# Kernel tuning notes

Measured on AMD Instinct MI355X. Metric: run time of the kernel, lower is better.

The kernel has to match this reference:

```python
import jax, jax.numpy as jnp
import numpy as np

N = 100000   # n_nodes
E = 800000   # n_edges
IN = 128
HID = 128
OUT = 40
EPS = 1e-5   # BatchNorm1d eps


def setup_inputs() -> dict:
    key = jax.random.key(0)
    ks = jax.random.split(key, 16)
    def w(k, i, o):
        return jax.random.normal(k, (i, o), jnp.float32) / np.sqrt(i).astype(np.float32)
    return {
        "x": jax.random.normal(ks[0], (N, IN), jnp.float32),
        "edge_index": jax.random.randint(ks[1], (2, E), 0, N, dtype=jnp.int64),
        # SAGEConv weights: Wl acts on aggregated neighbors, Wr on root features
        "Wl0": w(ks[2], IN, HID),  "Wr0": w(ks[3], IN, HID),
        "Wl1": w(ks[4], HID, HID), "Wr1": w(ks[5], HID, HID),
        "Wl2": w(ks[6], HID, OUT), "Wr2": w(ks[7], HID, OUT),
        "b2": jnp.zeros((OUT,), jnp.float32),  # bias only on last layer
        # BatchNorm params for layers 0,1 (last layer has no BN)
        "g0": jnp.ones((HID,), jnp.float32), "be0": jnp.zeros((HID,), jnp.float32),
        "g1": jnp.ones((HID,), jnp.float32), "be1": jnp.zeros((HID,), jnp.float32),
    }


def _sage_conv(x, src, dst, Wl, Wr, b=None):
    # mean aggregation of source messages at destination nodes
    msg = x[src]                                             # [E, d] gather
    agg = jax.ops.segment_sum(msg, dst, num_segments=N)      # [N, d]
    cnt = jax.ops.segment_sum(jnp.ones((src.shape[0],), x.dtype), dst,
                              num_segments=N)                # [N]
    mean = agg / jnp.maximum(cnt, 1.0)[:, None]
    out = mean @ Wl + x @ Wr
    if b is not None:
        out = out + b
    return out


def _batch_norm(h, gamma, beta):
    # training-mode BN over node dim, biased variance (matches torch BatchNorm1d)
    mu = h.mean(axis=0)
    var = h.var(axis=0)
    return (h - mu) * jax.lax.rsqrt(var + EPS) * gamma + beta


def reference(x, edge_index, Wl0, Wr0, Wl1, Wr1, Wl2, Wr2, b2, g0, be0, g1, be1):
    src, dst = edge_index[0], edge_index[1]
    h = _sage_conv(x, src, dst, Wl0, Wr0)
    h = jax.nn.relu(_batch_norm(h, g0, be0))
    h = _sage_conv(h, src, dst, Wl1, Wr1)
    h = jax.nn.relu(_batch_norm(h, g1, be1))
    h = _sage_conv(h, src, dst, Wl2, Wr2, b2)
    return h
```

## Files before the change

kernel.cpp:

```cpp
#include <hip/hip_runtime.h>
#include <hip/hip_bf16.h>

#define N_NODES 100000
#define N_EDGES 800000
#define EPS 1e-5f
#define NBANK 32
#define HB_BLOCKS 256
#define HB_PER 3125
#define CS_GPB 64
#define BUCKET_N 12500
#define MROW 68

typedef __attribute__((ext_vector_type(8))) short short8;
typedef __attribute__((ext_vector_type(4))) float floatx4;

__device__ __forceinline__ unsigned short f2b(float f) {
    unsigned int u = __float_as_uint(f);
    u = (u + 0x7fffu + ((u >> 16) & 1u)) >> 16;
    return (unsigned short)u;
}
__device__ __forceinline__ float blo(unsigned int u) { return __uint_as_float(u << 16); }
__device__ __forceinline__ float bhi(unsigned int u) { return __uint_as_float(u & 0xffff0000u); }

__global__ void cvt_f32_bf16(const float* __restrict__ x, unsigned short* __restrict__ o, int n4) {
    int i = blockIdx.x * blockDim.x + threadIdx.x;
    if (i >= n4) return;
    float4 v = ((const float4*)x)[i];
    ushort4 r;
    r.x = f2b(v.x); r.y = f2b(v.y); r.z = f2b(v.z); r.w = f2b(v.w);
    ((ushort4*)o)[i] = r;
}

__global__ void pack_w(const float* __restrict__ Wl, const float* __restrict__ Wr,
                       unsigned short* __restrict__ out, int Hreal, int NCT) {
    int tid = blockIdx.x * blockDim.x + threadIdx.x;
    int total = NCT * 8 * 64 * 8;
    if (tid >= total) return;
    int i = tid & 7;
    int lane = (tid >> 3) & 63;
    int q = tid >> 9;
    int c = q % NCT;
    int t = q / NCT;
    int k = t * 32 + (lane >> 4) * 8 + i;
    int n = c * 16 + (lane & 15);
    float v = 0.f;
    if (n < Hreal) v = (k < 128) ? Wl[k * Hreal + n] : Wr[(k - 128) * Hreal + n];
    out[tid] = f2b(v);
}

__global__ void __launch_bounds__(256) hist_k(const int* __restrict__ dst,
                                              unsigned int* __restrict__ cnt,
                                              unsigned int* __restrict__ bhist) {
    __shared__ unsigned int lh[8];
    if (threadIdx.x < 8) lh[threadIdx.x] = 0;
    __syncthreads();
    int start = blockIdx.x * HB_PER;
    for (int i = threadIdx.x; i < HB_PER; i += 256) {
        int d = dst[start + i];
        atomicAdd(&cnt[d], 1u);
        atomicAdd(&lh[(unsigned int)d / BUCKET_N], 1u);
    }
    __syncthreads();
    if (threadIdx.x < 8) bhist[threadIdx.x * HB_BLOCKS + blockIdx.x] = lh[threadIdx.x];
}

__global__ void bscan(unsigned int* __restrict__ A) {
    __shared__ unsigned int part[256];
    int t = threadIdx.x;
    unsigned int v[8];
    unsigned int s = 0;
#pragma unroll
    for (int i = 0; i < 8; i++) { v[i] = A[t * 8 + i]; s += v[i]; }
    part[t] = s; __syncthreads();
    for (int off = 1; off < 256; off <<= 1) {
        unsigned int add = (t >= off) ? part[t - off] : 0u;
        __syncthreads();
        part[t] += add;
        __syncthreads();
    }
    unsigned int base = part[t] - s;
#pragma unroll
    for (int i = 0; i < 8; i++) { unsigned int old = v[i]; A[t * 8 + i] = base; base += old; }
}

__global__ void __launch_bounds__(256) bscatter(const int* __restrict__ src,
                                                const int* __restrict__ dst,
                                                const unsigned int* __restrict__ boffs,
                                                unsigned int* __restrict__ ebuf) {
    __shared__ unsigned int cur[8];
    if (threadIdx.x < 8) cur[threadIdx.x] = boffs[threadIdx.x * HB_BLOCKS + blockIdx.x];
    __syncthreads();
    int start = blockIdx.x * HB_PER;
    for (int i = threadIdx.x; i < HB_PER; i += 256) {
        int d = dst[start + i];
        int s = src[start + i];
        unsigned int b = (unsigned int)d / BUCKET_N;
        unsigned int dl = (unsigned int)d - b * BUCKET_N;
        unsigned int pos = atomicAdd(&cur[b], 1u);
        ebuf[pos] = (unsigned int)s | (dl << 17);
    }
}

__global__ void __launch_bounds__(256) cscatter(const unsigned int* __restrict__ ebuf,
                                                const unsigned int* __restrict__ rowptr,
                                                unsigned int* __restrict__ cursor,
                                                int* __restrict__ srclist) {
    int g = blockIdx.x & 7;
    int gblk = blockIdx.x >> 3;
    unsigned int estart = rowptr[g * BUCKET_N];
    unsigned int eend = (g == 7) ? N_EDGES : rowptr[(g + 1) * BUCKET_N];
    unsigned int nume = eend - estart;
    unsigned int per = (nume + CS_GPB - 1) / CS_GPB;
    unsigned int s0 = estart + gblk * per;
    unsigned int s1 = s0 + per; if (s1 > eend) s1 = eend;
    unsigned int nodebase = g * BUCKET_N;
    for (unsigned int i = s0 + threadIdx.x; i < s1; i += 256) {
        unsigned int p = ebuf[i];
        unsigned int s = p & 0x1FFFFu;
        unsigned int node = nodebase + (p >> 17);
        unsigned int pos = atomicAdd(&cursor[node], 1u);
        srclist[pos] = (int)s;
    }
}

__global__ void scan1(const unsigned int* __restrict__ cnt, unsigned int* __restrict__ rowptr,
                      unsigned int* __restrict__ bsum) {
    __shared__ unsigned int sh[256];
    int t = threadIdx.x;
    int i = blockIdx.x * 256 + t;
    unsigned int v = (i < N_NODES) ? cnt[i] : 0u;
    sh[t] = v; __syncthreads();
    for (int off = 1; off < 256; off <<= 1) {
        unsigned int add = (t >= off) ? sh[t - off] : 0u;
        __syncthreads();
        sh[t] += add;
        __syncthreads();
    }
    if (i < N_NODES) rowptr[i] = sh[t] - v;
    if (t == 255) bsum[blockIdx.x] = sh[255];
}

__global__ void scan2(const unsigned int* __restrict__ bsum, unsigned int* __restrict__ boff, int nb) {
    __shared__ unsigned int sh[512];
    int t = threadIdx.x;
    unsigned int v = (t < nb) ? bsum[t] : 0u;
    sh[t] = v; __syncthreads();
    for (int off = 1; off < 512; off <<= 1) {
        unsigned int add = (t >= off) ? sh[t - off] : 0u;
        __syncthreads();
        sh[t] += add;
        __syncthreads();
    }
    if (t < nb) boff[t] = sh[t] - v;
}

__global__ void scan3(unsigned int* __restrict__ rowptr, const unsigned int* __restrict__ boff,
                      unsigned int* __restrict__ cursor) {
    int i = blockIdx.x * 256 + threadIdx.x;
    if (i < N_NODES) {
        unsigned int r = rowptr[i] + boff[blockIdx.x];
        rowptr[i] = r;
        cursor[i] = r;
    }
    if (i == N_NODES) rowptr[N_NODES] = N_EDGES;
}

__device__ __forceinline__ void agg_phase16(const unsigned short* __restrict__ hb,
                                            const unsigned int* __restrict__ rowptr,
                                            const int* __restrict__ srclist,
                                            unsigned int* __restrict__ smean,
                                            int wave, int g, int l, int blockrow) {
    const uint4* hp = (const uint4*)hb;
    int nl = wave * 4 + g;
    int node = blockrow + nl;
    float f0 = 0.f, f1 = 0.f, f2 = 0.f, f3 = 0.f, f4 = 0.f, f5 = 0.f, f6 = 0.f, f7 = 0.f;
    unsigned int b = rowptr[node], e = rowptr[node + 1];
    unsigned int p = b;
    for (; p + 4 <= e; p += 4) {
        int s0 = srclist[p];
        int s1 = srclist[p + 1];
        int s2 = srclist[p + 2];
        int s3 = srclist[p + 3];
        uint4 u0 = hp[(size_t)s0 * 16 + l];
        uint4 u1 = hp[(size_t)s1 * 16 + l];
        uint4 u2 = hp[(size_t)s2 * 16 + l];
        uint4 u3 = hp[(size_t)s3 * 16 + l];
        f0 += blo(u0.x); f1 += bhi(u0.x); f2 += blo(u0.y); f3 += bhi(u0.y);
        f4 += blo(u0.z); f5 += bhi(u0.z); f6 += blo(u0.w); f7 += bhi(u0.w);
        f0 += blo(u1.x); f1 += bhi(u1.x); f2 += blo(u1.y); f3 += bhi(u1.y);
        f4 += blo(u1.z); f5 += bhi(u1.z); f6 += blo(u1.w); f7 += bhi(u1.w);
        f0 += blo(u2.x); f1 += bhi(u2.x); f2 += blo(u2.y); f3 += bhi(u2.y);
        f4 += blo(u2.z); f5 += bhi(u2.z); f6 += blo(u2.w); f7 += bhi(u2.w);
        f0 += blo(u3.x); f1 += bhi(u3.x); f2 += blo(u3.y); f3 += bhi(u3.y);
        f4 += blo(u3.z); f5 += bhi(u3.z); f6 += blo(u3.w); f7 += bhi(u3.w);
    }
    if (p + 2 <= e) {
        int s0 = srclist[p];
        int s1 = srclist[p + 1];
        uint4 u0 = hp[(size_t)s0 * 16 + l];
        uint4 u1 = hp[(size_t)s1 * 16 + l];
        f0 += blo(u0.x); f1 += bhi(u0.x); f2 += blo(u0.y); f3 += bhi(u0.y);
        f4 += blo(u0.z); f5 += bhi(u0.z); f6 += blo(u0.w); f7 += bhi(u0.w);
        f0 += blo(u1.x); f1 += bhi(u1.x); f2 += blo(u1.y); f3 += bhi(u1.y);
        f4 += blo(u1.z); f5 += bhi(u1.z); f6 += blo(u1.w); f7 += bhi(u1.w);
        p += 2;
    }
    if (p < e) {
        int s0 = srclist[p];
        uint4 u0 = hp[(size_t)s0 * 16 + l];
        f0 += blo(u0.x); f1 += bhi(u0.x); f2 += blo(u0.y); f3 += bhi(u0.y);
        f4 += blo(u0.z); f5 += bhi(u0.z); f6 += blo(u0.w); f7 += bhi(u0.w);
    }
    unsigned int deg = e - b;
    float r = 1.0f / (float)(deg > 1u ? deg : 1u);
    uint4 o;
    o.x = (unsigned int)f2b(f0 * r) | ((unsigned int)f2b(f1 * r) << 16);
    o.y = (unsigned int)f2b(f2 * r) | ((unsigned int)f2b(f3 * r) << 16);
    o.z = (unsigned int)f2b(f4 * r) | ((unsigned int)f2b(f5 * r) << 16);
    o.w = (unsigned int)f2b(f6 * r) | ((unsigned int)f2b(f7 * r) << 16);
    *(uint4*)&smean[nl * MROW + l * 4] = o;
}

__global__ void __launch_bounds__(256) gemm2f_k(const unsigned short* __restrict__ hb,
                                                const unsigned int* __restrict__ rowptr,
                                                const int* __restrict__ srclist,
                                                const unsigned short* __restrict__ Bp,
                                                unsigned short* __restrict__ outb,
                                                float* __restrict__ sums) {
    __shared__ unsigned int smean[16 * MROW];
    __shared__ float lds_s[128];
    __shared__ float lds_s2[128];
    int wave = threadIdx.x >> 6;
    int lane = threadIdx.x & 63;
    int quad = lane >> 4;
    int l15 = lane & 15;
    int blockrow = blockIdx.x * 16;

    if (threadIdx.x < 128) { lds_s[threadIdx.x] = 0.f; lds_s2[threadIdx.x] = 0.f; }

    agg_phase16(hb, rowptr, srclist, smean, wave, quad, l15, blockrow);
    __syncthreads();

    floatx4 acc[2];
    acc[0] = (floatx4){0.f, 0.f, 0.f, 0.f};
    acc[1] = (floatx4){0.f, 0.f, 0.f, 0.f};

    int r0 = blockrow + l15;

#pragma unroll
    for (int t = 0; t < 8; t++) {
        short8 a0;
        if (t < 4) {
            a0 = *(const short8*)&smean[l15 * MROW + t * 16 + quad * 4];
        } else {
            int koff = (t & 3) * 32 + quad * 8;
            a0 = *(const short8*)(hb + (size_t)r0 * 128 + koff);
        }
#pragma unroll
        for (int c = 0; c < 2; c++) {
            int cidx = wave * 2 + c;
            short8 bf = *(const short8*)(Bp + ((size_t)(t * 8 + cidx) * 64 + lane) * 8);
            acc[c] = __builtin_amdgcn_mfma_f32_16x16x32_bf16(a0, bf, acc[c], 0, 0, 0);
        }
    }

#pragma unroll
    for (int c = 0; c < 2; c++) {
        int col = wave * 32 + c * 16 + l15;
        float s = 0.f, s2 = 0.f;
#pragma unroll
        for (int r = 0; r < 4; r++) {
            int row = blockrow + quad * 4 + r;
            float v = acc[c][r];
            outb[(size_t)row * 128 + col] = f2b(v);
            s += v; s2 += v * v;
        }
        s += __shfl_xor(s, 16);  s += __shfl_xor(s, 32);
        s2 += __shfl_xor(s2, 16); s2 += __shfl_xor(s2, 32);
        if (quad == 0) {
            atomicAdd(&lds_s[col], s);
            atomicAdd(&lds_s2[col], s2);
        }
    }

    __syncthreads();
    if (threadIdx.x < 128) {
        int bank = blockIdx.x & (NBANK - 1);
        atomicAdd(&sums[bank * 256 + threadIdx.x], lds_s[threadIdx.x]);
        atomicAdd(&sums[bank * 256 + 128 + threadIdx.x], lds_s2[threadIdx.x]);
    }
}

__global__ void __launch_bounds__(256) gemm3f_k(const unsigned short* __restrict__ hb,
                                                const unsigned int* __restrict__ rowptr,
                                                const int* __restrict__ srclist,
                                                const unsigned short* __restrict__ Bp,
                                                const float* __restrict__ bias,
                                                float* __restrict__ out) {
    __shared__ unsigned int smean[16 * MROW];
    int wave = threadIdx.x >> 6;
    int lane = threadIdx.x & 63;
    int quad = lane >> 4;
    int l15 = lane & 15;
    int blockrow = blockIdx.x * 16;

    agg_phase16(hb, rowptr, srclist, smean, wave, quad, l15, blockrow);
    __syncthreads();

    if (wave >= 3) return;

    floatx4 acc = (floatx4){0.f, 0.f, 0.f, 0.f};
    int r0 = blockrow + l15;

#pragma unroll
    for (int t = 0; t < 8; t++) {
        short8 a0;
        if (t < 4) {
            a0 = *(const short8*)&smean[l15 * MROW + t * 16 + quad * 4];
        } else {
            int koff = (t & 3) * 32 + quad * 8;
            a0 = *(const short8*)(hb + (size_t)r0 * 128 + koff);
        }
        short8 bf = *(const short8*)(Bp + ((size_t)(t * 3 + wave) * 64 + lane) * 8);
        acc = __builtin_amdgcn_mfma_f32_16x16x32_bf16(a0, bf, acc, 0, 0, 0);
    }

    int col = wave * 16 + l15;
    if (col < 40) {
#pragma unroll
        for (int r = 0; r < 4; r++) {
            int row = blockrow + quad * 4 + r;
            out[(size_t)row * 40 + col] = acc[r] + bias[col];
        }
    }
}

__global__ void bn_finalize(const float* __restrict__ sums, const float* __restrict__ g,
                            const float* __restrict__ be, float* __restrict__ sc,
                            float* __restrict__ sh) {
    __shared__ float lds[256];
    int t = threadIdx.x;
    float s = 0.f;
#pragma unroll 8
    for (int bk = 0; bk < NBANK; bk++) s += sums[bk * 256 + t];
    lds[t] = s;
    __syncthreads();
    if (t < 128) {
        float inv_n = 1.0f / (float)N_NODES;
        float mu = lds[t] * inv_n;
        float var = lds[128 + t] * inv_n - mu * mu;
        float sf = g[t] * rsqrtf(var + EPS);
        sc[t] = sf;
        sh[t] = be[t] - mu * sf;
    }
}

__global__ void bn_apply(const unsigned int* __restrict__ Cb, const float* __restrict__ sc,
                         const float* __restrict__ sh, unsigned short* __restrict__ ho) {
    int i = blockIdx.x * 256 + threadIdx.x;
    if (i >= N_NODES * 16) return;
    uint4 v = ((const uint4*)Cb)[i];
    int c0 = (i * 8) & 127;
    uint4 o;
    float e0 = fmaxf(0.f, blo(v.x) * sc[c0 + 0] + sh[c0 + 0]);
    float e1 = fmaxf(0.f, bhi(v.x) * sc[c0 + 1] + sh[c0 + 1]);
    float e2 = fmaxf(0.f, blo(v.y) * sc[c0 + 2] + sh[c0 + 2]);
    float e3 = fmaxf(0.f, bhi(v.y) * sc[c0 + 3] + sh[c0 + 3]);
    float e4 = fmaxf(0.f, blo(v.z) * sc[c0 + 4] + sh[c0 + 4]);
    float e5 = fmaxf(0.f, bhi(v.z) * sc[c0 + 5] + sh[c0 + 5]);
    float e6 = fmaxf(0.f, blo(v.w) * sc[c0 + 6] + sh[c0 + 6]);
    float e7 = fmaxf(0.f, bhi(v.w) * sc[c0 + 7] + sh[c0 + 7]);
    o.x = (unsigned int)f2b(e0) | ((unsigned int)f2b(e1) << 16);
    o.y = (unsigned int)f2b(e2) | ((unsigned int)f2b(e3) << 16);
    o.z = (unsigned int)f2b(e4) | ((unsigned int)f2b(e5) << 16);
    o.w = (unsigned int)f2b(e6) | ((unsigned int)f2b(e7) << 16);
    ((uint4*)ho)[i] = o;
}

extern "C" void kernel_launch(void* const* d_in, const int* in_sizes, int n_in,
                              void* d_out, int out_size, void* d_ws, size_t ws_size,
                              hipStream_t stream) {
    const float* x   = (const float*)d_in[0];
    const int* ei    = (const int*)d_in[1];
    const float* Wl0 = (const float*)d_in[2];
    const float* Wr0 = (const float*)d_in[3];
    const float* Wl1 = (const float*)d_in[4];
    const float* Wr1 = (const float*)d_in[5];
    const float* Wl2 = (const float*)d_in[6];
    const float* Wr2 = (const float*)d_in[7];
    const float* b2  = (const float*)d_in[8];
    const float* g0  = (const float*)d_in[9];
    const float* be0 = (const float*)d_in[10];
    const float* g1  = (const float*)d_in[11];
    const float* be1 = (const float*)d_in[12];

    char* ws = (char*)d_ws;
    size_t off = 0;
    auto alloc = [&](size_t bytes) -> void* {
        void* p = ws + off;
        off += (bytes + 4095) & ~(size_t)4095;
        return p;
    };

    const size_t NB16 = (size_t)N_NODES * 128 * 2;
    unsigned short* xb   = (unsigned short*)alloc(NB16);
    unsigned short* h1   = (unsigned short*)alloc(NB16);
    unsigned short* C    = (unsigned short*)alloc(NB16);
    unsigned int* cnt    = (unsigned int*)alloc((size_t)N_NODES * 4);
    unsigned int* rowptr = (unsigned int*)alloc((size_t)(N_NODES + 1) * 4);
    unsigned int* cursor = (unsigned int*)alloc((size_t)N_NODES * 4);
    int* srclist         = (int*)alloc((size_t)N_EDGES * 4);
    unsigned int* ebuf   = (unsigned int*)alloc((size_t)N_EDGES * 4);
    unsigned int* bhist  = (unsigned int*)alloc(8 * HB_BLOCKS * 4);
    unsigned int* bsum   = (unsigned int*)alloc(512 * 4);
    unsigned int* boff   = (unsigned int*)alloc(512 * 4);
    float* sums0         = (float*)alloc(NBANK * 256 * 4);
    float* sums1         = (float*)alloc(NBANK * 256 * 4);
    float* sc            = (float*)alloc(128 * 4);
    float* sh            = (float*)alloc(128 * 4);
    unsigned short* W0p  = (unsigned short*)alloc(8 * 8 * 64 * 8 * 2);
    unsigned short* W1p  = (unsigned short*)alloc(8 * 8 * 64 * 8 * 2);
    unsigned short* W2p  = (unsigned short*)alloc(3 * 8 * 64 * 8 * 2);
    unsigned short* h2   = xb;

    const int* srcp = ei;
    const int* dstp = ei + N_EDGES;

    hipMemsetAsync(cnt, 0, (size_t)N_NODES * 4, stream);
    hipMemsetAsync(sums0, 0, (size_t)2 * NBANK * 256 * 4, stream);
    cvt_f32_bf16<<<12500, 256, 0, stream>>>(x, xb, N_NODES * 32);
    pack_w<<<(8 * 4096 + 255) / 256, 256, 0, stream>>>(Wl0, Wr0, W0p, 128, 8);
    pack_w<<<(8 * 4096 + 255) / 256, 256, 0, stream>>>(Wl1, Wr1, W1p, 128, 8);
    pack_w<<<(3 * 4096 + 255) / 256, 256, 0, stream>>>(Wl2, Wr2, W2p, 40, 3);

    hist_k<<<HB_BLOCKS, 256, 0, stream>>>(dstp, cnt, bhist);
    scan1<<<391, 256, 0, stream>>>(cnt, rowptr, bsum);
    scan2<<<1, 512, 0, stream>>>(bsum, boff, 391);
    scan3<<<391, 256, 0, stream>>>(rowptr, boff, cursor);
    bscan<<<1, 256, 0, stream>>>(bhist);
    bscatter<<<HB_BLOCKS, 256, 0, stream>>>(srcp, dstp, bhist, ebuf);
    cscatter<<<8 * CS_GPB, 256, 0, stream>>>(ebuf, rowptr, cursor, srclist);

    gemm2f_k<<<6250, 256, 0, stream>>>(xb, rowptr, srclist, W0p, C, sums0);
    bn_finalize<<<1, 256, 0, stream>>>(sums0, g0, be0, sc, sh);
    bn_apply<<<6250, 256, 0, stream>>>((const unsigned int*)C, sc, sh, h1);

    gemm2f_k<<<6250, 256, 0, stream>>>(h1, rowptr, srclist, W1p, C, sums1);
    bn_finalize<<<1, 256, 0, stream>>>(sums1, g1, be1, sc, sh);
    bn_apply<<<6250, 256, 0, stream>>>((const unsigned int*)C, sc, sh, h2);

    gemm3f_k<<<6250, 256, 0, stream>>>(h2, rowptr, srclist, W2p, b2, (float*)d_out);

    (void)in_sizes; (void)n_in; (void)out_size; (void)ws_size;
}
```

Baseline: 372.1 us.

## Balance neighbor aggregation by splitting block edges evenly across lane groups

The mean aggregation now gives each 16-lane group an equal slice of the block's 16-node edge range instead of one destination node per group. The local destination index is packed into the upper bits of srclist, so partial sums can be flushed with LDS float atomics into a per-block fp32 accumulator before normalisation and the bf16 conversion. This targets the load imbalance from skewed node degrees, where one group with many edges stalls the whole block. In exchange it adds an LDS zeroing pass, an extra barrier, shuffles to broadcast edge indices, and LDS atomic traffic at each destination change.

```diff
diff --git a/kernel.cpp b/kernel.cpp
--- a/kernel.cpp
+++ b/kernel.cpp
@@ -10,6 +10,7 @@
 #define CS_GPB 64
 #define BUCKET_N 12500
 #define MROW 68
+#define ACC_S 132
 
 typedef __attribute__((ext_vector_type(8))) short short8;
 typedef __attribute__((ext_vector_type(4))) float floatx4;
@@ -119,7 +120,7 @@
         unsigned int s = p & 0x1FFFFu;
         unsigned int node = nodebase + (p >> 17);
         unsigned int pos = atomicAdd(&cursor[node], 1u);
-        srclist[pos] = (int)s;
+        srclist[pos] = (int)(s | ((node & 15u) << 17));
     }
 }
 
@@ -168,57 +169,91 @@
 __device__ __forceinline__ void agg_phase16(const unsigned short* __restrict__ hb,
                                             const unsigned int* __restrict__ rowptr,
                                             const int* __restrict__ srclist,
+                                            float* __restrict__ accf,
                                             unsigned int* __restrict__ smean,
-                                            int wave, int g, int l, int blockrow) {
+                                            int blockrow) {
+    const int tid = threadIdx.x;
+    const int g = tid >> 4;
+    const int l = tid & 15;
+    const int srcbase = (g & 3) << 4;
+
+    for (int i = tid; i < 16 * ACC_S; i += 256) accf[i] = 0.f;
+    __syncthreads();
+
+    unsigned int e0 = rowptr[blockrow];
+    unsigned int e1 = rowptr[blockrow + 16];
+    unsigned int nE = e1 - e0;
+    unsigned int per = (nE + 15u) >> 4;
+    unsigned int start = e0 + (unsigned int)g * per;
+    unsigned int end = start + per;
+    if (end > e1) end = e1;
+
     const uint4* hp = (const uint4*)hb;
-    int nl = wave * 4 + g;
-    int node = blockrow + nl;
     float f0 = 0.f, f1 = 0.f, f2 = 0.f, f3 = 0.f, f4 = 0.f, f5 = 0.f, f6 = 0.f, f7 = 0.f;
-    unsigned int b = rowptr[node], e = rowptr[node + 1];
-    unsigned int p = b;
-    for (; p + 4 <= e; p += 4) {
-        int s0 = srclist[p];
-        int s1 = srclist[p + 1];
-        int s2 = srclist[p + 2];
-        int s3 = srclist[p + 3];
-        uint4 u0 = hp[(size_t)s0 * 16 + l];
-        uint4 u1 = hp[(size_t)s1 * 16 + l];
-        uint4 u2 = hp[(size_t)s2 * 16 + l];
-        uint4 u3 = hp[(size_t)s3 * 16 + l];
-        f0 += blo(u0.x); f1 += bhi(u0.x); f2 += blo(u0.y); f3 += bhi(u0.y);
-        f4 += blo(u0.z); f5 += bhi(u0.z); f6 += blo(u0.w); f7 += bhi(u0.w);
-        f0 += blo(u1.x); f1 += bhi(u1.x); f2 += blo(u1.y); f3 += bhi(u1.y);
-        f4 += blo(u1.z); f5 += bhi(u1.z); f6 += blo(u1.w); f7 += bhi(u1.w);
-        f0 += blo(u2.x); f1 += bhi(u2.x); f2 += blo(u2.y); f3 += bhi(u2.y);
-        f4 += blo(u2.z); f5 += bhi(u2.z); f6 += blo(u2.w); f7 += bhi(u2.w);
-        f0 += blo(u3.x); f1 += bhi(u3.x); f2 += blo(u3.y); f3 += bhi(u3.y);
-        f4 += blo(u3.z); f5 += bhi(u3.z); f6 += blo(u3.w); f7 += bhi(u3.w);
-    }
-    if (p + 2 <= e) {
-        int s0 = srclist[p];
-        int s1 = srclist[p + 1];
-        uint4 u0 = hp[(size_t)s0 * 16 + l];
-        uint4 u1 = hp[(size_t)s1 * 16 + l];
-        f0 += blo(u0.x); f1 += bhi(u0.x); f2 += blo(u0.y); f3 += bhi(u0.y);
-        f4 += blo(u0.z); f5 += bhi(u0.z); f6 += blo(u0.w); f7 += bhi(u0.w);
-        f0 += blo(u1.x); f1 += bhi(u1.x); f2 += blo(u1.y); f3 += bhi(u1.y);
-        f4 += blo(u1.z); f5 += bhi(u1.z); f6 += blo(u1.w); f7 += bhi(u1.w);
-        p += 2;
-    }
-    if (p < e) {
-        int s0 = srclist[p];
-        uint4 u0 = hp[(size_t)s0 * 16 + l];
-        f0 += blo(u0.x); f1 += bhi(u0.x); f2 += blo(u0.y); f3 += bhi(u0.y);
-        f4 += blo(u0.z); f5 += bhi(u0.z); f6 += blo(u0.w); f7 += bhi(u0.w);
-    }
-    unsigned int deg = e - b;
-    float r = 1.0f / (float)(deg > 1u ? deg : 1u);
-    uint4 o;
-    o.x = (unsigned int)f2b(f0 * r) | ((unsigned int)f2b(f1 * r) << 16);
-    o.y = (unsigned int)f2b(f2 * r) | ((unsigned int)f2b(f3 * r) << 16);
-    o.z = (unsigned int)f2b(f4 * r) | ((unsigned int)f2b(f5 * r) << 16);
-    o.w = (unsigned int)f2b(f6 * r) | ((unsigned int)f2b(f7 * r) << 16);
-    *(uint4*)&smean[nl * MROW + l * 4] = o;
+    int dcur = -1;
+
+#define ACC8(U) { f0 += blo(U.x); f1 += bhi(U.x); f2 += blo(U.y); f3 += bhi(U.y); \
+                  f4 += blo(U.z); f5 += bhi(U.z); f6 += blo(U.w); f7 += bhi(U.w); }
+#define FLUSHA() { if (dcur >= 0) { float* ap = accf + dcur * ACC_S + l * 8; \
+    atomicAdd(&ap[(0 + l) & 7], f0); atomicAdd(&ap[(1 + l) & 7], f1); \
+    atomicAdd(&ap[(2 + l) & 7], f2); atomicAdd(&ap[(3 + l) & 7], f3); \
+    atomicAdd(&ap[(4 + l) & 7], f4); atomicAdd(&ap[(5 + l) & 7], f5); \
+    atomicAdd(&ap[(6 + l) & 7], f6); atomicAdd(&ap[(7 + l) & 7], f7); \
+    f0 = f1 = f2 = f3 = f4 = f5 = f6 = f7 = 0.f; } }
+#define EDGE(P, U) { int dd = (int)((P >> 17) & 15u); \
+    if (dd != dcur) { FLUSHA(); dcur = dd; } ACC8(U); }
+
+    for (unsigned int base = start; base < end; base += 16u) {
+        unsigned int rem = end - base;
+        int m = rem < 16u ? (int)rem : 16;
+        unsigned int pk = 0u;
+        if ((unsigned int)l < rem) pk = (unsigned int)srclist[base + (unsigned int)l];
+        int j = 0;
+        for (; j + 4 <= m; j += 4) {
+            unsigned int p0 = (unsigned int)__shfl((int)pk, srcbase + j + 0);
+            unsigned int p1 = (unsigned int)__shfl((int)pk, srcbase + j + 1);
+            unsigned int p2 = (unsigned int)__shfl((int)pk, srcbase + j + 2);
+            unsigned int p3 = (unsigned int)__shfl((int)pk, srcbase + j + 3);
+            uint4 u0 = hp[(size_t)(p0 & 0x1FFFFu) * 16 + l];
+            uint4 u1 = hp[(size_t)(p1 & 0x1FFFFu) * 16 + l];
+            uint4 u2 = hp[(size_t)(p2 & 0x1FFFFu) * 16 + l];
+            uint4 u3 = hp[(size_t)(p3 & 0x1FFFFu) * 16 + l];
+            EDGE(p0, u0); EDGE(p1, u1); EDGE(p2, u2); EDGE(p3, u3);
+        }
+        for (; j < m; ++j) {
+            unsigned int p0 = (unsigned int)__shfl((int)pk, srcbase + j);
+            uint4 u0 = hp[(size_t)(p0 & 0x1FFFFu) * 16 + l];
+            EDGE(p0, u0);
+        }
+    }
+    FLUSHA();
+#undef EDGE
+#undef FLUSHA
+#undef ACC8
+
+    __syncthreads();
+
+    {
+        unsigned int b = rowptr[blockrow + g];
+        unsigned int e = rowptr[blockrow + g + 1];
+        unsigned int deg = e - b;
+        float r = 1.0f / (float)(deg > 1u ? deg : 1u);
+        const float* ap = accf + g * ACC_S + l * 8;
+        float v0 = ap[(0 + l) & 7] * r;
+        float v1 = ap[(1 + l) & 7] * r;
+        float v2 = ap[(2 + l) & 7] * r;
+        float v3 = ap[(3 + l) & 7] * r;
+        float v4 = ap[(4 + l) & 7] * r;
+        float v5 = ap[(5 + l) & 7] * r;
+        float v6 = ap[(6 + l) & 7] * r;
+        float v7 = ap[(7 + l) & 7] * r;
+        uint4 o;
+        o.x = (unsigned int)f2b(v0) | ((unsigned int)f2b(v1) << 16);
+        o.y = (unsigned int)f2b(v2) | ((unsigned int)f2b(v3) << 16);
+        o.z = (unsigned int)f2b(v4) | ((unsigned int)f2b(v5) << 16);
+        o.w = (unsigned int)f2b(v6) | ((unsigned int)f2b(v7) << 16);
+        *(uint4*)&smean[g * MROW + l * 4] = o;
+    }
 }
 
 __global__ void __launch_bounds__(256) gemm2f_k(const unsigned short* __restrict__ hb,
@@ -227,6 +262,7 @@
                                                 const unsigned short* __restrict__ Bp,
                                                 unsigned short* __restrict__ outb,
                                                 float* __restrict__ sums) {
+    __shared__ float accf[16 * ACC_S];
     __shared__ unsigned int smean[16 * MROW];
     __shared__ float lds_s[128];
     __shared__ float lds_s2[128];
@@ -238,7 +274,7 @@
 
     if (threadIdx.x < 128) { lds_s[threadIdx.x] = 0.f; lds_s2[threadIdx.x] = 0.f; }
 
-    agg_phase16(hb, rowptr, srclist, smean, wave, quad, l15, blockrow);
+    agg_phase16(hb, rowptr, srclist, accf, smean, blockrow);
     __syncthreads();
 
     floatx4 acc[2];
@@ -297,6 +333,7 @@
                                                 const unsigned short* __restrict__ Bp,
                                                 const float* __restrict__ bias,
                                                 float* __restrict__ out) {
+    __shared__ float accf[16 * ACC_S];
     __shared__ unsigned int smean[16 * MROW];
     int wave = threadIdx.x >> 6;
     int lane = threadIdx.x & 63;
@@ -304,7 +341,7 @@
     int l15 = lane & 15;
     int blockrow = blockIdx.x * 16;
 
-    agg_phase16(hb, rowptr, srclist, smean, wave, quad, l15, blockrow);
+    agg_phase16(hb, rowptr, srclist, accf, smean, blockrow);
     __syncthreads();
 
     if (wave >= 3) return;
```

After: 645.7 us. 73.5% more time.

## Sort nodes by degree so each aggregation block handles similar-degree nodes

Applied to the files above, without the earlier changes.

Adds a counting sort of nodes by in-degree (capped at 63) into a permutation. The fused aggregate+GEMM kernels then process blocks of 16 nodes taken from that permutation rather than 16 consecutive nodes, which balances the per-wave gather loop lengths. It also unrolls the neighbor gather to 8 loads per step and adds an occupancy hint to launch_bounds. The cost is three extra small kernels, indirect row indexing, and scattered output writes and root-feature reads that lose locality.

```diff
diff --git a/kernel.cpp b/kernel.cpp
--- a/kernel.cpp
+++ b/kernel.cpp
@@ -165,52 +165,109 @@
     if (i == N_NODES) rowptr[N_NODES] = N_EDGES;
 }
 
+__global__ void __launch_bounds__(256) deg_hist(const unsigned int* __restrict__ cnt,
+                                                unsigned int* __restrict__ dh) {
+    __shared__ unsigned int lh[64];
+    if (threadIdx.x < 64) lh[threadIdx.x] = 0;
+    __syncthreads();
+    int i = blockIdx.x * 256 + threadIdx.x;
+    if (i < N_NODES) {
+        unsigned int d = cnt[i]; if (d > 63u) d = 63u;
+        atomicAdd(&lh[d], 1u);
+    }
+    __syncthreads();
+    if (threadIdx.x < 64 && lh[threadIdx.x]) atomicAdd(&dh[threadIdx.x], lh[threadIdx.x]);
+}
+
+__global__ void deg_scan(unsigned int* __restrict__ dh, unsigned int* __restrict__ dcur) {
+    int t = threadIdx.x;
+    unsigned int v = dh[t];
+    unsigned int s = v;
+#pragma unroll
+    for (int off = 1; off < 64; off <<= 1) {
+        unsigned int n = __shfl_up(s, off);
+        if (t >= off) s += n;
+    }
+    unsigned int ex = s - v;
+    dh[t] = ex;
+    dcur[t] = ex;
+}
+
+__global__ void __launch_bounds__(256) deg_scatter(const unsigned int* __restrict__ cnt,
+                                                   unsigned int* __restrict__ dcur,
+                                                   int* __restrict__ perm) {
+    __shared__ unsigned int lh[64];
+    __shared__ unsigned int lbase[64];
+    int t = threadIdx.x;
+    if (t < 64) lh[t] = 0;
+    __syncthreads();
+    int i = blockIdx.x * 256 + t;
+    unsigned int d = 0, loc = 0;
+    bool valid = i < N_NODES;
+    if (valid) {
+        d = cnt[i]; if (d > 63u) d = 63u;
+        loc = atomicAdd(&lh[d], 1u);
+    }
+    __syncthreads();
+    if (t < 64 && lh[t]) lbase[t] = atomicAdd(&dcur[t], lh[t]);
+    __syncthreads();
+    if (valid) perm[lbase[d] + loc] = i;
+}
+
 __device__ __forceinline__ void agg_phase16(const unsigned short* __restrict__ hb,
                                             const unsigned int* __restrict__ rowptr,
                                             const int* __restrict__ srclist,
                                             unsigned int* __restrict__ smean,
-                                            int wave, int g, int l, int blockrow) {
+                                            const int* __restrict__ pblk,
+                                            int wave, int g, int l) {
     const uint4* hp = (const uint4*)hb;
     int nl = wave * 4 + g;
-    int node = blockrow + nl;
+    int node = pblk[nl];
     float f0 = 0.f, f1 = 0.f, f2 = 0.f, f3 = 0.f, f4 = 0.f, f5 = 0.f, f6 = 0.f, f7 = 0.f;
     unsigned int b = rowptr[node], e = rowptr[node + 1];
     unsigned int p = b;
-    for (; p + 4 <= e; p += 4) {
-        int s0 = srclist[p];
-        int s1 = srclist[p + 1];
-        int s2 = srclist[p + 2];
-        int s3 = srclist[p + 3];
+#define ACC8(U) { f0 += blo(U.x); f1 += bhi(U.x); f2 += blo(U.y); f3 += bhi(U.y); \
+                  f4 += blo(U.z); f5 += bhi(U.z); f6 += blo(U.w); f7 += bhi(U.w); }
+    for (; p + 8 <= e; p += 8) {
+        int s0 = srclist[p];     int s1 = srclist[p + 1];
+        int s2 = srclist[p + 2]; int s3 = srclist[p + 3];
+        int s4 = srclist[p + 4]; int s5 = srclist[p + 5];
+        int s6 = srclist[p + 6]; int s7 = srclist[p + 7];
         uint4 u0 = hp[(size_t)s0 * 16 + l];
         uint4 u1 = hp[(size_t)s1 * 16 + l];
         uint4 u2 = hp[(size_t)s2 * 16 + l];
         uint4 u3 = hp[(size_t)s3 * 16 + l];
-        f0 += blo(u0.x); f1 += bhi(u0.x); f2 += blo(u0.y); f3 += bhi(u0.y);
-        f4 += blo(u0.z); f5 += bhi(u0.z); f6 += blo(u0.w); f7 += bhi(u0.w);
-        f0 += blo(u1.x); f1 += bhi(u1.x); f2 += blo(u1.y); f3 += bhi(u1.y);
-        f4 += blo(u1.z); f5 += bhi(u1.z); f6 += blo(u1.w); f7 += bhi(u1.w);
-        f0 += blo(u2.x); f1 += bhi(u2.x); f2 += blo(u2.y); f3 += bhi(u2.y);
-        f4 += blo(u2.z); f5 += bhi(u2.z); f6 += blo(u2.w); f7 += bhi(u2.w);
-        f0 += blo(u3.x); f1 += bhi(u3.x); f2 += blo(u3.y); f3 += bhi(u3.y);
-        f4 += blo(u3.z); f5 += bhi(u3.z); f6 += blo(u3.w); f7 += bhi(u3.w);
+        uint4 u4 = hp[(size_t)s4 * 16 + l];
+        uint4 u5 = hp[(size_t)s5 * 16 + l];
+        uint4 u6 = hp[(size_t)s6 * 16 + l];
+        uint4 u7 = hp[(size_t)s7 * 16 + l];
+        ACC8(u0); ACC8(u1); ACC8(u2); ACC8(u3);
+        ACC8(u4); ACC8(u5); ACC8(u6); ACC8(u7);
+    }
+    if (p + 4 <= e) {
+        int s0 = srclist[p];     int s1 = srclist[p + 1];
+        int s2 = srclist[p + 2]; int s3 = srclist[p + 3];
+        uint4 u0 = hp[(size_t)s0 * 16 + l];
+        uint4 u1 = hp[(size_t)s1 * 16 + l];
+        uint4 u2 = hp[(size_t)s2 * 16 + l];
+        uint4 u3 = hp[(size_t)s3 * 16 + l];
+        ACC8(u0); ACC8(u1); ACC8(u2); ACC8(u3);
+        p += 4;
     }
     if (p + 2 <= e) {
         int s0 = srclist[p];
         int s1 = srclist[p + 1];
         uint4 u0 = hp[(size_t)s0 * 16 + l];
         uint4 u1 = hp[(size_t)s1 * 16 + l];
-        f0 += blo(u0.x); f1 += bhi(u0.x); f2 += blo(u0.y); f3 += bhi(u0.y);
-        f4 += blo(u0.z); f5 += bhi(u0.z); f6 += blo(u0.w); f7 += bhi(u0.w);
-        f0 += blo(u1.x); f1 += bhi(u1.x); f2 += blo(u1.y); f3 += bhi(u1.y);
-        f4 += blo(u1.z); f5 += bhi(u1.z); f6 += blo(u1.w); f7 += bhi(u1.w);
+        ACC8(u0); ACC8(u1);
         p += 2;
     }
     if (p < e) {
         int s0 = srclist[p];
         uint4 u0 = hp[(size_t)s0 * 16 + l];
-        f0 += blo(u0.x); f1 += bhi(u0.x); f2 += blo(u0.y); f3 += bhi(u0.y);
-        f4 += blo(u0.z); f5 += bhi(u0.z); f6 += blo(u0.w); f7 += bhi(u0.w);
-    }
+        ACC8(u0);
+    }
+#undef ACC8
     unsigned int deg = e - b;
     float r = 1.0f / (float)(deg > 1u ? deg : 1u);
     uint4 o;
@@ -221,31 +278,34 @@
     *(uint4*)&smean[nl * MROW + l * 4] = o;
 }
 
-__global__ void __launch_bounds__(256) gemm2f_k(const unsigned short* __restrict__ hb,
-                                                const unsigned int* __restrict__ rowptr,
-                                                const int* __restrict__ srclist,
-                                                const unsigned short* __restrict__ Bp,
-                                                unsigned short* __restrict__ outb,
-                                                float* __restrict__ sums) {
+__global__ void __launch_bounds__(256, 8) gemm2f_k(const unsigned short* __restrict__ hb,
+                                                   const unsigned int* __restrict__ rowptr,
+                                                   const int* __restrict__ srclist,
+                                                   const int* __restrict__ perm,
+                                                   const unsigned short* __restrict__ Bp,
+                                                   unsigned short* __restrict__ outb,
+                                                   float* __restrict__ sums) {
     __shared__ unsigned int smean[16 * MROW];
     __shared__ float lds_s[128];
     __shared__ float lds_s2[128];
+    __shared__ int pblk[16];
     int wave = threadIdx.x >> 6;
     int lane = threadIdx.x & 63;
     int quad = lane >> 4;
     int l15 = lane & 15;
-    int blockrow = blockIdx.x * 16;
 
     if (threadIdx.x < 128) { lds_s[threadIdx.x] = 0.f; lds_s2[threadIdx.x] = 0.f; }
-
-    agg_phase16(hb, rowptr, srclist, smean, wave, quad, l15, blockrow);
+    if (threadIdx.x < 16) pblk[threadIdx.x] = perm[blockIdx.x * 16 + threadIdx.x];
+    __syncthreads();
+
+    agg_phase16(hb, rowptr, srclist, smean, pblk, wave, quad, l15);
     __syncthreads();
 
     floatx4 acc[2];
     acc[0] = (floatx4){0.f, 0.f, 0.f, 0.f};
     acc[1] = (floatx4){0.f, 0.f, 0.f, 0.f};
 
-    int r0 = blockrow + l15;
+    int r0 = pblk[l15];
 
 #pragma unroll
     for (int t = 0; t < 8; t++) {
@@ -270,7 +330,7 @@
         float s = 0.f, s2 = 0.f;
 #pragma unroll
         for (int r = 0; r < 4; r++) {
-            int row = blockrow + quad * 4 + r;
+            int row = pblk[quad * 4 + r];
             float v = acc[c][r];
             outb[(size_t)row * 128 + col] = f2b(v);
             s += v; s2 += v * v;
@@ -291,26 +351,30 @@
     }
 }
 
-__global__ void __launch_bounds__(256) gemm3f_k(const unsigned short* __restrict__ hb,
-                                                const unsigned int* __restrict__ rowptr,
-                                                const int* __restrict__ srclist,
-                                                const unsigned short* __restrict__ Bp,
-                                                const float* __restrict__ bias,
-                                                float* __restrict__ out) {
+__global__ void __launch_bounds__(256, 8) gemm3f_k(const unsigned short* __restrict__ hb,
+                                                   const unsigned int* __restrict__ rowptr,
+                                                   const int* __restrict__ srclist,
+                                                   const int* __restrict__ perm,
+                                                   const unsigned short* __restrict__ Bp,
+                                                   const float* __restrict__ bias,
+                                                   float* __restrict__ out) {
     __shared__ unsigned int smean[16 * MROW];
+    __shared__ int pblk[16];
     int wave = threadIdx.x >> 6;
     int lane = threadIdx.x & 63;
     int quad = lane >> 4;
     int l15 = lane & 15;
-    int blockrow = blockIdx.x * 16;
-
-    agg_phase16(hb, rowptr, srclist, smean, wave, quad, l15, blockrow);
+
+    if (threadIdx.x < 16) pblk[threadIdx.x] = perm[blockIdx.x * 16 + threadIdx.x];
+    __syncthreads();
+
+    agg_phase16(hb, rowptr, srclist, smean, pblk, wave, quad, l15);
     __syncthreads();
 
     if (wave >= 3) return;
 
     floatx4 acc = (floatx4){0.f, 0.f, 0.f, 0.f};
-    int r0 = blockrow + l15;
+    int r0 = pblk[l15];
 
 #pragma unroll
     for (int t = 0; t < 8; t++) {
@@ -329,7 +393,7 @@
     if (col < 40) {
 #pragma unroll
         for (int r = 0; r < 4; r++) {
-            int row = blockrow + quad * 4 + r;
+            int row = pblk[quad * 4 + r];
             out[(size_t)row * 40 + col] = acc[r] + bias[col];
         }
     }
@@ -421,12 +485,16 @@
     unsigned short* W0p  = (unsigned short*)alloc(8 * 8 * 64 * 8 * 2);
     unsigned short* W1p  = (unsigned short*)alloc(8 * 8 * 64 * 8 * 2);
     unsigned short* W2p  = (unsigned short*)alloc(3 * 8 * 64 * 8 * 2);
+    unsigned int* dh     = (unsigned int*)alloc(64 * 4);
+    unsigned int* dcur   = (unsigned int*)alloc(64 * 4);
+    int* perm            = (int*)alloc((size_t)N_NODES * 4);
     unsigned short* h2   = xb;
 
     const int* srcp = ei;
     const int* dstp = ei + N_EDGES;
 
     hipMemsetAsync(cnt, 0, (size_t)N_NODES * 4, stream);
+    hipMemsetAsync(dh, 0, 64 * 4, stream);
     hipMemsetAsync(sums0, 0, (size_t)2 * NBANK * 256 * 4, stream);
     cvt_f32_bf16<<<12500, 256, 0, stream>>>(x, xb, N_NODES * 32);
     pack_w<<<(8 * 4096 + 255) / 256, 256, 0, stream>>>(Wl0, Wr0, W0p, 128, 8);
@@ -441,15 +509,19 @@
     bscatter<<<HB_BLOCKS, 256, 0, stream>>>(srcp, dstp, bhist, ebuf);
     cscatter<<<8 * CS_GPB, 256, 0, stream>>>(ebuf, rowptr, cursor, srclist);
 
-    gemm2f_k<<<6250, 256, 0, stream>>>(xb, rowptr, srclist, W0p, C, sums0);
+    deg_hist<<<391, 256, 0, stream>>>(cnt, dh);
+    deg_scan<<<1, 64, 0, stream>>>(dh, dcur);
+    deg_scatter<<<391, 256, 0, stream>>>(cnt, dcur, perm);
+
+    gemm2f_k<<<6250, 256, 0, stream>>>(xb, rowptr, srclist, perm, W0p, C, sums0);
     bn_finalize<<<1, 256, 0, stream>>>(sums0, g0, be0, sc, sh);
     bn_apply<<<6250, 256, 0, stream>>>((const unsigned int*)C, sc, sh, h1);
 
-    gemm2f_k<<<6250, 256, 0, stream>>>(h1, rowptr, srclist, W1p, C, sums1);
+    gemm2f_k<<<6250, 256, 0, stream>>>(h1, rowptr, srclist, perm, W1p, C, sums1);
     bn_finalize<<<1, 256, 0, stream>>>(sums1, g1, be1, sc, sh);
     bn_apply<<<6250, 256, 0, stream>>>((const unsigned int*)C, sc, sh, h2);
 
-    gemm3f_k<<<6250, 256, 0, stream>>>(h2, rowptr, srclist, W2p, b2, (float*)d_out);
+    gemm3f_k<<<6250, 256, 0, stream>>>(h2, rowptr, srclist, perm, W2p, b2, (float*)d_out);
 
     (void)in_sizes; (void)n_in; (void)out_size; (void)ws_size;
 }
```

Result: slower. 449.1 us (+20.7%).

## Fuse BN+ReLU into gather, reorder last layer to transform-then-aggregate

Applied to the files above, without the earlier changes.

Drops both bn_apply passes. The BatchNorm scale/shift and ReLU are now applied on the fly, both when neighbor rows are gathered during aggregation and when root rows are loaded for the GEMM. The last SAGE layer is reordered: a dense kernel first multiplies the activated features by Wl2 and Wr2, and a new kernel then aggregates the 40-wide (padded to 64) projected rows. Gather traffic in the final layer shrinks from 128 to 64 bf16 columns per edge. In exchange, BN arithmetic is recomputed for every edge visit, and the bf16 rounding order changes in the last layer.

```diff
diff --git a/kernel.cpp b/kernel.cpp
--- a/kernel.cpp
+++ b/kernel.cpp
@@ -21,6 +21,9 @@
 }
 __device__ __forceinline__ float blo(unsigned int u) { return __uint_as_float(u << 16); }
 __device__ __forceinline__ float bhi(unsigned int u) { return __uint_as_float(u & 0xffff0000u); }
+__device__ __forceinline__ float b2f(unsigned short s) {
+    return __uint_as_float(((unsigned int)s) << 16);
+}
 
 __global__ void cvt_f32_bf16(const float* __restrict__ x, unsigned short* __restrict__ o, int n4) {
     int i = blockIdx.x * blockDim.x + threadIdx.x;
@@ -165,17 +168,44 @@
     if (i == N_NODES) rowptr[N_NODES] = N_EDGES;
 }
 
+template<int BN>
 __device__ __forceinline__ void agg_phase16(const unsigned short* __restrict__ hb,
                                             const unsigned int* __restrict__ rowptr,
                                             const int* __restrict__ srclist,
                                             unsigned int* __restrict__ smean,
+                                            const float* __restrict__ sc,
+                                            const float* __restrict__ sh,
                                             int wave, int g, int l, int blockrow) {
     const uint4* hp = (const uint4*)hb;
     int nl = wave * 4 + g;
     int node = blockrow + nl;
     float f0 = 0.f, f1 = 0.f, f2 = 0.f, f3 = 0.f, f4 = 0.f, f5 = 0.f, f6 = 0.f, f7 = 0.f;
+    float sc0r = 0.f, sc1r = 0.f, sc2r = 0.f, sc3r = 0.f, sc4r = 0.f, sc5r = 0.f, sc6r = 0.f, sc7r = 0.f;
+    float sh0r = 0.f, sh1r = 0.f, sh2r = 0.f, sh3r = 0.f, sh4r = 0.f, sh5r = 0.f, sh6r = 0.f, sh7r = 0.f;
+    if (BN) {
+        const float* s0 = sc + l * 8;
+        const float* s1 = sh + l * 8;
+        sc0r = s0[0]; sc1r = s0[1]; sc2r = s0[2]; sc3r = s0[3];
+        sc4r = s0[4]; sc5r = s0[5]; sc6r = s0[6]; sc7r = s0[7];
+        sh0r = s1[0]; sh1r = s1[1]; sh2r = s1[2]; sh3r = s1[3];
+        sh4r = s1[4]; sh5r = s1[5]; sh6r = s1[6]; sh7r = s1[7];
+    }
     unsigned int b = rowptr[node], e = rowptr[node + 1];
     unsigned int p = b;
+#define ACC8(U) { \
+    if (BN) { \
+        f0 += fmaxf(0.f, fmaf(blo(U.x), sc0r, sh0r)); \
+        f1 += fmaxf(0.f, fmaf(bhi(U.x), sc1r, sh1r)); \
+        f2 += fmaxf(0.f, fmaf(blo(U.y), sc2r, sh2r)); \
+        f3 += fmaxf(0.f, fmaf(bhi(U.y), sc3r, sh3r)); \
+        f4 += fmaxf(0.f, fmaf(blo(U.z), sc4r, sh4r)); \
+        f5 += fmaxf(0.f, fmaf(bhi(U.z), sc5r, sh5r)); \
+        f6 += fmaxf(0.f, fmaf(blo(U.w), sc6r, sh6r)); \
+        f7 += fmaxf(0.f, fmaf(bhi(U.w), sc7r, sh7r)); \
+    } else { \
+        f0 += blo(U.x); f1 += bhi(U.x); f2 += blo(U.y); f3 += bhi(U.y); \
+        f4 += blo(U.z); f5 += bhi(U.z); f6 += blo(U.w); f7 += bhi(U.w); \
+    } }
     for (; p + 4 <= e; p += 4) {
         int s0 = srclist[p];
         int s1 = srclist[p + 1];
@@ -185,32 +215,22 @@
         uint4 u1 = hp[(size_t)s1 * 16 + l];
         uint4 u2 = hp[(size_t)s2 * 16 + l];
         uint4 u3 = hp[(size_t)s3 * 16 + l];
-        f0 += blo(u0.x); f1 += bhi(u0.x); f2 += blo(u0.y); f3 += bhi(u0.y);
-        f4 += blo(u0.z); f5 += bhi(u0.z); f6 += blo(u0.w); f7 += bhi(u0.w);
-        f0 += blo(u1.x); f1 += bhi(u1.x); f2 += blo(u1.y); f3 += bhi(u1.y);
-        f4 += blo(u1.z); f5 += bhi(u1.z); f6 += blo(u1.w); f7 += bhi(u1.w);
-        f0 += blo(u2.x); f1 += bhi(u2.x); f2 += blo(u2.y); f3 += bhi(u2.y);
-        f4 += blo(u2.z); f5 += bhi(u2.z); f6 += blo(u2.w); f7 += bhi(u2.w);
-        f0 += blo(u3.x); f1 += bhi(u3.x); f2 += blo(u3.y); f3 += bhi(u3.y);
-        f4 += blo(u3.z); f5 += bhi(u3.z); f6 += blo(u3.w); f7 += bhi(u3.w);
+        ACC8(u0); ACC8(u1); ACC8(u2); ACC8(u3);
     }
     if (p + 2 <= e) {
         int s0 = srclist[p];
         int s1 = srclist[p + 1];
         uint4 u0 = hp[(size_t)s0 * 16 + l];
         uint4 u1 = hp[(size_t)s1 * 16 + l];
-        f0 += blo(u0.x); f1 += bhi(u0.x); f2 += blo(u0.y); f3 += bhi(u0.y);
-        f4 += blo(u0.z); f5 += bhi(u0.z); f6 += blo(u0.w); f7 += bhi(u0.w);
-        f0 += blo(u1.x); f1 += bhi(u1.x); f2 += blo(u1.y); f3 += bhi(u1.y);
-        f4 += blo(u1.z); f5 += bhi(u1.z); f6 += blo(u1.w); f7 += bhi(u1.w);
+        ACC8(u0); ACC8(u1);
         p += 2;
     }
     if (p < e) {
         int s0 = srclist[p];
         uint4 u0 = hp[(size_t)s0 * 16 + l];
-        f0 += blo(u0.x); f1 += bhi(u0.x); f2 += blo(u0.y); f3 += bhi(u0.y);
-        f4 += blo(u0.z); f5 += bhi(u0.z); f6 += blo(u0.w); f7 += bhi(u0.w);
-    }
+        ACC8(u0);
+    }
+#undef ACC8
     unsigned int deg = e - b;
     float r = 1.0f / (float)(deg > 1u ? deg : 1u);
     uint4 o;
@@ -221,24 +241,45 @@
     *(uint4*)&smean[nl * MROW + l * 4] = o;
 }
 
+__device__ __forceinline__ short8 bn_pack8(short8 raw, const float* __restrict__ scb,
+                                           const float* __restrict__ shb, int koff) {
+    short8 r;
+#pragma unroll
+    for (int i = 0; i < 8; i++) {
+        float v = b2f((unsigned short)raw[i]);
+        v = fmaxf(0.f, fmaf(v, scb[koff + i], shb[koff + i]));
+        r[i] = (short)f2b(v);
+    }
+    return r;
+}
+
+template<int BN>
 __global__ void __launch_bounds__(256) gemm2f_k(const unsigned short* __restrict__ hb,
                                                 const unsigned int* __restrict__ rowptr,
                                                 const int* __restrict__ srclist,
+                                                const float* __restrict__ sc,
+                                                const float* __restrict__ sh,
                                                 const unsigned short* __restrict__ Bp,
                                                 unsigned short* __restrict__ outb,
                                                 float* __restrict__ sums) {
     __shared__ unsigned int smean[16 * MROW];
     __shared__ float lds_s[128];
     __shared__ float lds_s2[128];
+    __shared__ float scb[128];
+    __shared__ float shb[128];
     int wave = threadIdx.x >> 6;
     int lane = threadIdx.x & 63;
     int quad = lane >> 4;
     int l15 = lane & 15;
     int blockrow = blockIdx.x * 16;
 
-    if (threadIdx.x < 128) { lds_s[threadIdx.x] = 0.f; lds_s2[threadIdx.x] = 0.f; }
-
-    agg_phase16(hb, rowptr, srclist, smean, wave, quad, l15, blockrow);
+    if (threadIdx.x < 128) {
+        lds_s[threadIdx.x] = 0.f; lds_s2[threadIdx.x] = 0.f;
+        if (BN) { scb[threadIdx.x] = sc[threadIdx.x]; shb[threadIdx.x] = sh[threadIdx.x]; }
+    }
+    if (BN) __syncthreads();
+
+    agg_phase16<BN>(hb, rowptr, srclist, smean, sc, sh, wave, quad, l15, blockrow);
     __syncthreads();
 
     floatx4 acc[2];
@@ -254,7 +295,8 @@
             a0 = *(const short8*)&smean[l15 * MROW + t * 16 + quad * 4];
         } else {
             int koff = (t & 3) * 32 + quad * 8;
-            a0 = *(const short8*)(hb + (size_t)r0 * 128 + koff);
+            short8 raw = *(const short8*)(hb + (size_t)r0 * 128 + koff);
+            a0 = BN ? bn_pack8(raw, scb, shb, koff) : raw;
         }
 #pragma unroll
         for (int c = 0; c < 2; c++) {
@@ -291,47 +333,119 @@
     }
 }
 
-__global__ void __launch_bounds__(256) gemm3f_k(const unsigned short* __restrict__ hb,
-                                                const unsigned int* __restrict__ rowptr,
-                                                const int* __restrict__ srclist,
-                                                const unsigned short* __restrict__ Bp,
-                                                const float* __restrict__ bias,
-                                                float* __restrict__ out) {
-    __shared__ unsigned int smean[16 * MROW];
+__global__ void __launch_bounds__(256) dense_k(const unsigned short* __restrict__ hb,
+                                               const float* __restrict__ sc,
+                                               const float* __restrict__ sh,
+                                               const unsigned short* __restrict__ Bp,
+                                               const float* __restrict__ bias,
+                                               unsigned short* __restrict__ P,
+                                               float* __restrict__ Q) {
+    __shared__ float scb[128];
+    __shared__ float shb[128];
     int wave = threadIdx.x >> 6;
     int lane = threadIdx.x & 63;
     int quad = lane >> 4;
     int l15 = lane & 15;
     int blockrow = blockIdx.x * 16;
 
-    agg_phase16(hb, rowptr, srclist, smean, wave, quad, l15, blockrow);
-    __syncthreads();
-
-    if (wave >= 3) return;
-
-    floatx4 acc = (floatx4){0.f, 0.f, 0.f, 0.f};
+    if (threadIdx.x < 128) { scb[threadIdx.x] = sc[threadIdx.x]; shb[threadIdx.x] = sh[threadIdx.x]; }
+    __syncthreads();
+
     int r0 = blockrow + l15;
-
-#pragma unroll
-    for (int t = 0; t < 8; t++) {
-        short8 a0;
-        if (t < 4) {
-            a0 = *(const short8*)&smean[l15 * MROW + t * 16 + quad * 4];
-        } else {
-            int koff = (t & 3) * 32 + quad * 8;
-            a0 = *(const short8*)(hb + (size_t)r0 * 128 + koff);
-        }
-        short8 bf = *(const short8*)(Bp + ((size_t)(t * 3 + wave) * 64 + lane) * 8);
-        acc = __builtin_amdgcn_mfma_f32_16x16x32_bf16(a0, bf, acc, 0, 0, 0);
-    }
-
-    int col = wave * 16 + l15;
-    if (col < 40) {
+    short8 af[4];
+#pragma unroll
+    for (int t = 0; t < 4; t++) {
+        int koff = t * 32 + quad * 8;
+        short8 raw = *(const short8*)(hb + (size_t)r0 * 128 + koff);
+        af[t] = bn_pack8(raw, scb, shb, koff);
+    }
+
+    if (wave < 3) {
+        floatx4 aP = (floatx4){0.f, 0.f, 0.f, 0.f};
+        floatx4 aQ = (floatx4){0.f, 0.f, 0.f, 0.f};
+#pragma unroll
+        for (int t = 0; t < 4; t++) {
+            short8 bl = *(const short8*)(Bp + ((size_t)(t * 3 + wave) * 64 + lane) * 8);
+            aP = __builtin_amdgcn_mfma_f32_16x16x32_bf16(af[t], bl, aP, 0, 0, 0);
+        }
+#pragma unroll
+        for (int t = 0; t < 4; t++) {
+            short8 br = *(const short8*)(Bp + ((size_t)((t + 4) * 3 + wave) * 64 + lane) * 8);
+            aQ = __builtin_amdgcn_mfma_f32_16x16x32_bf16(af[t], br, aQ, 0, 0, 0);
+        }
+        int col = wave * 16 + l15;
 #pragma unroll
         for (int r = 0; r < 4; r++) {
             int row = blockrow + quad * 4 + r;
-            out[(size_t)row * 40 + col] = acc[r] + bias[col];
-        }
+            P[(size_t)row * 64 + col] = f2b(aP[r]);
+        }
+        if (col < 40) {
+#pragma unroll
+            for (int r = 0; r < 4; r++) {
+                int row = blockrow + quad * 4 + r;
+                Q[(size_t)row * 40 + col] = aQ[r] + bias[col];
+            }
+        }
+    } else {
+#pragma unroll
+        for (int r = 0; r < 4; r++) {
+            int row = blockrow + quad * 4 + r;
+            P[(size_t)row * 64 + 48 + l15] = 0;
+        }
+    }
+}
+
+__global__ void __launch_bounds__(256) agg40_k(const unsigned short* __restrict__ P,
+                                               const unsigned int* __restrict__ rowptr,
+                                               const int* __restrict__ srclist,
+                                               const float* __restrict__ Q,
+                                               float* __restrict__ out) {
+    int tid = threadIdx.x;
+    int g = tid >> 3;
+    int l = tid & 7;
+    int node = blockIdx.x * 32 + g;
+    const uint4* pp = (const uint4*)P;
+    float f0 = 0.f, f1 = 0.f, f2 = 0.f, f3 = 0.f, f4 = 0.f, f5 = 0.f, f6 = 0.f, f7 = 0.f;
+    unsigned int b = rowptr[node], e = rowptr[node + 1];
+    unsigned int p = b;
+#define ACC8(U) { f0 += blo(U.x); f1 += bhi(U.x); f2 += blo(U.y); f3 += bhi(U.y); \
+                  f4 += blo(U.z); f5 += bhi(U.z); f6 += blo(U.w); f7 += bhi(U.w); }
+    for (; p + 4 <= e; p += 4) {
+        int s0 = srclist[p];
+        int s1 = srclist[p + 1];
+        int s2 = srclist[p + 2];
+        int s3 = srclist[p + 3];
+        uint4 u0 = pp[(size_t)s0 * 8 + l];
+        uint4 u1 = pp[(size_t)s1 * 8 + l];
+        uint4 u2 = pp[(size_t)s2 * 8 + l];
+        uint4 u3 = pp[(size_t)s3 * 8 + l];
+        ACC8(u0); ACC8(u1); ACC8(u2); ACC8(u3);
+    }
+    if (p + 2 <= e) {
+        int s0 = srclist[p];
+        int s1 = srclist[p + 1];
+        uint4 u0 = pp[(size_t)s0 * 8 + l];
+        uint4 u1 = pp[(size_t)s1 * 8 + l];
+        ACC8(u0); ACC8(u1);
+        p += 2;
+    }
+    if (p < e) {
+        int s0 = srclist[p];
+        uint4 u0 = pp[(size_t)s0 * 8 + l];
+        ACC8(u0);
+    }
+#undef ACC8
+    unsigned int deg = e - b;
+    float r = 1.0f / (float)(deg > 1u ? deg : 1u);
+    if (l < 5) {
+        size_t base = (size_t)node * 40 + l * 8;
+        float4 o1, o2;
+        o1.x = f0 * r + Q[base + 0]; o1.y = f1 * r + Q[base + 1];
+        o1.z = f2 * r + Q[base + 2]; o1.w = f3 * r + Q[base + 3];
+        o2.x = f4 * r + Q[base + 4]; o2.y = f5 * r + Q[base + 5];
+        o2.z = f6 * r + Q[base + 6]; o2.w = f7 * r + Q[base + 7];
+        *(float4*)(out + base) = o1;
+        *(float4*)(out + base + 4) = o2;
     }
 }
 
@@ -353,28 +467,6 @@
         sc[t] = sf;
         sh[t] = be[t] - mu * sf;
     }
-}
-
-__global__ void bn_apply(const unsigned int* __restrict__ Cb, const float* __restrict__ sc,
-                         const float* __restrict__ sh, unsigned short* __restrict__ ho) {
-    int i = blockIdx.x * 256 + threadIdx.x;
-    if (i >= N_NODES * 16) return;
-    uint4 v = ((const uint4*)Cb)[i];
-    int c0 = (i * 8) & 127;
-    uint4 o;
-    float e0 = fmaxf(0.f, blo(v.x) * sc[c0 + 0] + sh[c0 + 0]);
-    float e1 = fmaxf(0.f, bhi(v.x) * sc[c0 + 1] + sh[c0 + 1]);
-    float e2 = fmaxf(0.f, blo(v.y) * sc[c0 + 2] + sh[c0 + 2]);
-    float e3 = fmaxf(0.f, bhi(v.y) * sc[c0 + 3] + sh[c0 + 3]);
-    float e4 = fmaxf(0.f, blo(v.z) * sc[c0 + 4] + sh[c0 + 4]);
-    float e5 = fmaxf(0.f, bhi(v.z) * sc[c0 + 5] + sh[c0 + 5]);
-    float e6 = fmaxf(0.f, blo(v.w) * sc[c0 + 6] + sh[c0 + 6]);
-    float e7 = fmaxf(0.f, bhi(v.w) * sc[c0 + 7] + sh[c0 + 7]);
-    o.x = (unsigned int)f2b(e0) | ((unsigned int)f2b(e1) << 16);
-    o.y = (unsigned int)f2b(e2) | ((unsigned int)f2b(e3) << 16);
-    o.z = (unsigned int)f2b(e4) | ((unsigned int)f2b(e5) << 16);
-    o.w = (unsigned int)f2b(e6) | ((unsigned int)f2b(e7) << 16);
-    ((uint4*)ho)[i] = o;
 }
 
 extern "C" void kernel_launch(void* const* d_in, const int* in_sizes, int n_in,
@@ -404,8 +496,8 @@
 
     const size_t NB16 = (size_t)N_NODES * 128 * 2;
     unsigned short* xb   = (unsigned short*)alloc(NB16);
-    unsigned short* h1   = (unsigned short*)alloc(NB16);
-    unsigned short* C    = (unsigned short*)alloc(NB16);
+    unsigned short* C0b  = (unsigned short*)alloc(NB16);
+    unsigned short* C1b  = (unsigned short*)alloc(NB16);
     unsigned int* cnt    = (unsigned int*)alloc((size_t)N_NODES * 4);
     unsigned int* rowptr = (unsigned int*)alloc((size_t)(N_NODES + 1) * 4);
     unsigned int* cursor = (unsigned int*)alloc((size_t)N_NODES * 4);
@@ -421,7 +513,9 @@
     unsigned short* W0p  = (unsigned short*)alloc(8 * 8 * 64 * 8 * 2);
     unsigned short* W1p  = (unsigned short*)alloc(8 * 8 * 64 * 8 * 2);
     unsigned short* W2p  = (unsigned short*)alloc(3 * 8 * 64 * 8 * 2);
-    unsigned short* h2   = xb;
+
+    unsigned short* P64  = C0b;
+    float* Q             = (float*)xb;
 
     const int* srcp = ei;
     const int* dstp = ei + N_EDGES;
@@ -441,15 +535,14 @@
     bscatter<<<HB_BLOCKS, 256, 0, stream>>>(srcp, dstp, bhist, ebuf);
     cscatter<<<8 * CS_GPB, 256, 0, stream>>>(ebuf, rowptr, cursor, srclist);
 
-    gemm2f_k<<<6250, 256, 0, stream>>>(xb, rowptr, srclist, W0p, C, sums0);
+    gemm2f_k<0><<<6250, 256, 0, stream>>>(xb, rowptr, srclist, nullptr, nullptr, W0p, C0b, sums0);
     bn_finalize<<<1, 256, 0, stream>>>(sums0, g0, be0, sc, sh);
-    bn_apply<<<6250, 256, 0, stream>>>((const unsigned int*)C, sc, sh, h1);
-
-    gemm2f_k<<<6250, 256, 0, stream>>>(h1, rowptr, srclist, W1p, C, sums1);
+
+    gemm2f_k<1><<<6250, 256, 0, stream>>>(C0b, rowptr, srclist, sc, sh, W1p, C1b, sums1);
     bn_finalize<<<1, 256, 0, stream>>>(sums1, g1, be1, sc, sh);
-    bn_apply<<<6250, 256, 0, stream>>>((const unsigned int*)C, sc, sh, h2);
-
-    gemm3f_k<<<6250, 256, 0, stream>>>(h2, rowptr, srclist, W2p, b2, (float*)d_out);
+
+    dense_k<<<6250, 256, 0, stream>>>(C1b, sc, sh, W2p, b2, P64, Q);
+    agg40_k<<<3125, 256, 0, stream>>>(P64, rowptr, srclist, Q, (float*)d_out);
 
     (void)in_sizes; (void)n_in; (void)out_size; (void)ws_size;
 }
```

After: 360.6 us. 3.1% less time.
